# Kernel tuning notes

Measured on AMD Instinct MI355X. Metric: run time of the kernel, lower is better.

## Reference

```python
import jax, jax.numpy as jnp
import numpy as np

D_IN = 1024
D_H = 1024

def setup_inputs() -> dict:
    key = jax.random.key(0)
    ks = jax.random.split(key, 9)
    s = 1.0 / np.sqrt(D_IN)
    inp = {
        'x': jax.random.normal(ks[0], (4, 2048, D_IN), dtype=jnp.float32),
        'wq': jax.random.uniform(ks[1], (D_IN, D_H), jnp.float32, -s, s),
        'bq': jax.random.uniform(ks[2], (D_H,), jnp.float32, -s, s),
        'wk': jax.random.uniform(ks[3], (D_IN, D_H), jnp.float32, -s, s),
        'bk': jax.random.uniform(ks[4], (D_H,), jnp.float32, -s, s),
        'wv': jax.random.uniform(ks[5], (D_IN, D_H), jnp.float32, -s, s),
        'bv': jax.random.uniform(ks[6], (D_H,), jnp.float32, -s, s),
        'wo': jax.random.uniform(ks[7], (D_H, D_IN), jnp.float32, -s, s),
        'bo': jax.random.uniform(ks[8], (D_IN,), jnp.float32, -s, s),
    }
    return inp

def reference(x, wq, bq, wk, bk, wv, bv, wo, bo):
    # q,k,v: [b, s, d]
    q = x @ wq + bq
    k = x @ wk + bk
    v = x @ wv + bv
    scale = 1.0 / jnp.sqrt(jnp.asarray(D_H, x.dtype))
    attn = jnp.einsum('bqd,bkd->bqk', q, k) * scale  # [b, s, s]
    attn = jax.nn.softmax(attn, axis=-1)
    score = jnp.einsum('bqk,bkd->bqd', attn, v)
    out = score @ wo + bo
    return out
```

## Files before the change

### kernel.cpp

```cpp
#include <hip/hip_runtime.h>


typedef unsigned short u16;
typedef short bf16x8 __attribute__((ext_vector_type(8)));
typedef float f32x4 __attribute__((ext_vector_type(4)));

#define SEQ 2048
#define DIM 1024

__device__ __forceinline__ u16 f2bf(float f) {
    unsigned u = __builtin_bit_cast(unsigned, f);
    u += 0x7fffu + ((u >> 16) & 1u);
    return (u16)(u >> 16);
}

__device__ __forceinline__ void async16(void* lds, const void* gmem) {
    __builtin_amdgcn_global_load_lds(
        (const __attribute__((address_space(1))) void*)gmem,
        (__attribute__((address_space(3))) void*)lds, 16, 0, 0);
}

__global__ __launch_bounds__(256) void cast_x_kernel(
    const float* __restrict__ x, u16* __restrict__ xb,
    const float* __restrict__ bq, const float* __restrict__ bk,
    const float* __restrict__ bv, float* __restrict__ bqkv,
    float* __restrict__ l)
{
    const int b = blockIdx.x;
    if (b < 8192) {
        const int idx = b * 256 + threadIdx.x;
        float4 v = ((const float4*)x)[idx];
        ushort4 o;
        o.x = f2bf(v.x); o.y = f2bf(v.y); o.z = f2bf(v.z); o.w = f2bf(v.w);
        ((ushort4*)xb)[idx] = o;
    } else {
        const int i = (b - 8192) * 256 + threadIdx.x;
        if (i < 3072)
            bqkv[i] = (i < 1024) ? bq[i] : (i < 2048) ? bk[i - 1024] : bv[i - 2048];
        else if (i < 3072 + 8192)
            l[i - 3072] = 0.f;
    }
}

__global__ __launch_bounds__(256) void transpose_cast_all(
    const float* __restrict__ W0, const float* __restrict__ W1,
    const float* __restrict__ W2, const float* __restrict__ W3,
    u16* __restrict__ Tqkv, u16* __restrict__ To)
{
    __shared__ float tile[32][33];
    const int z = blockIdx.z;
    const float* W = (z == 0) ? W0 : (z == 1) ? W1 : (z == 2) ? W2 : W3;
    u16* T = (z < 3) ? (Tqkv + (size_t)z * 1048576) : To;

    const int bx = blockIdx.x * 32, by = blockIdx.y * 32;
    const int tx = threadIdx.x, ty = threadIdx.y;
    #pragma unroll
    for (int r = 0; r < 4; ++r)
        tile[ty + r * 8][tx] = W[(size_t)(by + ty + r * 8) * DIM + bx + tx];
    __syncthreads();
    #pragma unroll
    for (int r = 0; r < 4; ++r) {
        const float v = tile[tx][ty + r * 8];
        T[(size_t)(bx + ty + r * 8) * DIM + by + tx] = f2bf(v);
    }
}

#define EPI_BF16BIAS 0
#define EPI_BF16     1
#define EPI_ELOGIT   2
#define EPI_PVOUT    3

template<int EPI, int K, int LDA, int LDB, int LDC>
__global__ __launch_bounds__(128, 2) void gemm2w(
    const u16* __restrict__ A, const u16* __restrict__ Bt,
    const float* __restrict__ bias, u16* __restrict__ C,
    float* __restrict__ Cf, float* __restrict__ lsum,
    float scale, long sA, long sB, long sC)
{
    __shared__ u16 sA0[128 * 32], sB0[128 * 32];
    __shared__ u16 sA1[128 * 32], sB1[128 * 32];

    const int z = blockIdx.z;
    A  += (size_t)z * sA;
    Bt += (size_t)z * sB;

    const int t  = threadIdx.x;
    const int m0 = blockIdx.y * 128, n0 = blockIdx.x * 128;
    const int wv = t >> 6, lane = t & 63;
    const int wm = wv * 64;
    const int lrow = lane & 15, quad = lane >> 4;
    const int sw = quad ^ ((lrow >> 1) & 3);

    f32x4 acc[4][8];
    #pragma unroll
    for (int i = 0; i < 4; ++i)
        #pragma unroll
        for (int j = 0; j < 8; ++j)
            acc[i][j] = (f32x4){0.f, 0.f, 0.f, 0.f};

    auto stage = [&](u16* dA, u16* dB, int k0) {
        #pragma unroll
        for (int p = 0; p < 4; ++p) {
            const int slot = p * 128 + t;
            const int row  = slot >> 2;
            const int c8   = (slot & 3) ^ ((row >> 1) & 3);
            async16(&dA[slot * 8], &A[(size_t)(m0 + row) * LDA + k0 + c8 * 8]);
        }
        #pragma unroll
        for (int p = 0; p < 4; ++p) {
            const int slot = p * 128 + t;
            const int row  = slot >> 2;
            const int c8   = (slot & 3) ^ ((row >> 1) & 3);
            async16(&dB[slot * 8], &Bt[(size_t)(n0 + row) * LDB + k0 + c8 * 8]);
        }
    };
    auto compute = [&](const u16* bA, const u16* bB) {
        bf16x8 af[4], bf[8];
        #pragma unroll
        for (int i = 0; i < 4; ++i)
            af[i] = *(const bf16x8*)&bA[((wm + i * 16 + lrow) * 4 + sw) * 8];
        #pragma unroll
        for (int j = 0; j < 8; ++j)
            bf[j] = *(const bf16x8*)&bB[((j * 16 + lrow) * 4 + sw) * 8];
        #pragma unroll
        for (int i = 0; i < 4; ++i)
            #pragma unroll
            for (int j = 0; j < 8; ++j)
                acc[i][j] = __builtin_amdgcn_mfma_f32_16x16x32_bf16(
                    af[i], bf[j], acc[i][j], 0, 0, 0);
    };

    stage(sA0, sB0, 0);
    __syncthreads();
    #pragma unroll 1
    for (int k0 = 0; k0 + 64 < K; k0 += 64) {
        stage(sA1, sB1, k0 + 32);
        compute(sA0, sB0);
        __syncthreads();
        stage(sA0, sB0, k0 + 64);
        compute(sA1, sB1);
        __syncthreads();
    }
    stage(sA1, sB1, K - 32);
    compute(sA0, sB0);
    __syncthreads();
    compute(sA1, sB1);

    if (EPI == EPI_PVOUT) Cf += (size_t)z * sC;
    else                  C  += (size_t)z * sC;

    #pragma unroll
    for (int i = 0; i < 4; ++i) {
        const int row = m0 + wm + i * 16 + quad * 4;
        if (EPI == EPI_BF16BIAS) {
            #pragma unroll
            for (int j = 0; j < 8; ++j) {
                const int col = n0 + j * 16 + lrow;
                const float b = bias[col];
                const f32x4 a = acc[i][j];
                #pragma unroll
                for (int r = 0; r < 4; ++r)
                    C[(size_t)(row + r) * LDC + col] = f2bf(a[r] + b);
            }
        } else if (EPI == EPI_BF16) {
            #pragma unroll
            for (int j = 0; j < 8; ++j) {
                const int col = n0 + j * 16 + lrow;
                const f32x4 a = acc[i][j];
                #pragma unroll
                for (int r = 0; r < 4; ++r)
                    C[(size_t)(row + r) * LDC + col] = f2bf(a[r]);
            }
        } else if (EPI == EPI_ELOGIT) {
            float rs[4] = {0.f, 0.f, 0.f, 0.f};
            #pragma unroll
            for (int j = 0; j < 8; ++j) {
                const int col = n0 + j * 16 + lrow;
                const f32x4 a = acc[i][j];
                #pragma unroll
                for (int r = 0; r < 4; ++r) {
                    const float e = __expf(a[r] * scale);
                    C[(size_t)(row + r) * LDC + col] = f2bf(e);
                    rs[r] += e;
                }
            }
            #pragma unroll
            for (int r = 0; r < 4; ++r) {
                float s = rs[r];
                s += __shfl_xor(s, 1, 64);
                s += __shfl_xor(s, 2, 64);
                s += __shfl_xor(s, 4, 64);
                s += __shfl_xor(s, 8, 64);
                if (lrow == 0)
                    atomicAdd(&lsum[(size_t)z * 2048 + row + r], s);
            }
        } else {
            float linv[4];
            #pragma unroll
            for (int r = 0; r < 4; ++r)
                linv[r] = 1.0f / lsum[(size_t)z * 2048 + row + r];
            #pragma unroll
            for (int j = 0; j < 8; ++j) {
                const int col = n0 + j * 16 + lrow;
                const float b = bias[col];
                const f32x4 a = acc[i][j];
                #pragma unroll
                for (int r = 0; r < 4; ++r)
                    Cf[(size_t)(row + r) * LDC + col] = a[r] * linv[r] + b;
            }
        }
    }
}

extern "C" void kernel_launch(void* const* d_in, const int* in_sizes, int n_in,
                              void* d_out, int out_size, void* d_ws, size_t ws_size,
                              hipStream_t stream)
{
    const float* x  = (const float*)d_in[0];
    const float* wq = (const float*)d_in[1];
    const float* bq = (const float*)d_in[2];
    const float* wk = (const float*)d_in[3];
    const float* bk = (const float*)d_in[4];
    const float* wv = (const float*)d_in[5];
    const float* bv = (const float*)d_in[6];
    const float* wo = (const float*)d_in[7];
    const float* bo = (const float*)d_in[8];
    float* out = (float*)d_out;

    u16* w16   = (u16*)d_ws;
    u16* xb    = w16;
    u16* qkv   = w16 + 8388608;
    u16* E     = w16 + 33554432;
    u16* wqkvT = w16 + 50331648;
    u16* woT   = w16 + 53477376;
    float* bqkv = (float*)(w16 + 54525952);
    float* l    = (float*)(w16 + 54532096);
    u16* VWoT  = w16;

    const u16* q_ = qkv;
    const u16* k_ = qkv + 1024;
    const u16* v_ = qkv + 2048;

    cast_x_kernel<<<8236, dim3(256), 0, stream>>>(x, xb, bq, bk, bv, bqkv, l);
    transpose_cast_all<<<dim3(32, 32, 4), dim3(32, 8), 0, stream>>>(
        wq, wk, wv, wo, wqkvT, woT);

    gemm2w<EPI_BF16BIAS, 1024, 1024, 1024, 3072>
        <<<dim3(24, 64, 1), dim3(128), 0, stream>>>(
            xb, wqkvT, bqkv, qkv, nullptr, nullptr, 1.f, 0, 0, 0);

    gemm2w<EPI_ELOGIT, 1024, 3072, 3072, 2048>
        <<<dim3(16, 16, 4), dim3(128), 0, stream>>>(
            q_, k_, nullptr, E, nullptr, l, 0.03125f,
            6291456, 6291456, 4194304);

    gemm2w<EPI_BF16, 1024, 1024, 3072, 2048>
        <<<dim3(16, 8, 4), dim3(128), 0, stream>>>(
            woT, v_, nullptr, VWoT, nullptr, nullptr, 1.f,
            0, 6291456, 2097152);

    gemm2w<EPI_PVOUT, 2048, 2048, 2048, 1024>
        <<<dim3(8, 16, 4), dim3(128), 0, stream>>>(
            E, VWoT, bo, nullptr, out, l, 1.f,
            4194304, 2097152, 2097152);
}
```

Baseline: 305.5 us.

## Rewrite GEMM as 8-wave 256x256 tile kernel with staged async pipeline

The 2-wave 128x128 GEMM is replaced by an 8-wave kernel computing 256x256 output tiles with K=64 steps. Global-to-LDS copies are split into four half-tile stages, issued two tiles ahead and interleaved with four MFMA quadrants separated by barriers, with explicit vmcnt waits and s_setprio around the MFMA bursts. LDS uses an XOR swizzle. The goal is more reuse per loaded tile and better overlap of memory with matrix math. In exchange, grids shrink (e.g. 128-256 blocks), which may underfill the GPU's CUs, and the many barriers add synchronization overhead.

```diff
diff --git a/kernel.cpp b/kernel.cpp
--- a/kernel.cpp
+++ b/kernel.cpp
@@ -70,103 +70,162 @@
 #define EPI_ELOGIT   2
 #define EPI_PVOUT    3
 
+#define FENCE() asm volatile("" ::: "memory")
+
+#define MFMA_QUAD(mh, nh)                                                    \
+    do {                                                                     \
+        __builtin_amdgcn_s_setprio(1);                                       \
+        _Pragma("unroll")                                                    \
+        for (int ks = 0; ks < 2; ++ks)                                       \
+            _Pragma("unroll")                                                \
+            for (int q = 0; q < 4; ++q)                                      \
+                _Pragma("unroll")                                            \
+                for (int nn = 0; nn < 2; ++nn)                               \
+                    acc[(mh) * 4 + q][(nh) * 2 + nn] =                       \
+                        __builtin_amdgcn_mfma_f32_16x16x32_bf16(             \
+                            aF[q][ks], bF[(nh) * 2 + nn][ks],                \
+                            acc[(mh) * 4 + q][(nh) * 2 + nn], 0, 0, 0);      \
+        __builtin_amdgcn_s_setprio(0);                                       \
+    } while (0)
+
 template<int EPI, int K, int LDA, int LDB, int LDC>
-__global__ __launch_bounds__(128, 2) void gemm2w(
+__global__ __launch_bounds__(512, 2) void gemm8w(
     const u16* __restrict__ A, const u16* __restrict__ Bt,
     const float* __restrict__ bias, u16* __restrict__ C,
     float* __restrict__ Cf, float* __restrict__ lsum,
     float scale, long sA, long sB, long sC)
 {
-    __shared__ u16 sA0[128 * 32], sB0[128 * 32];
-    __shared__ u16 sA1[128 * 32], sB1[128 * 32];
+    __shared__ u16 lds[2][2][2][8192];
+
+    constexpr int NT = K / 64;
 
     const int z = blockIdx.z;
     A  += (size_t)z * sA;
     Bt += (size_t)z * sB;
 
-    const int t  = threadIdx.x;
-    const int m0 = blockIdx.y * 128, n0 = blockIdx.x * 128;
-    const int wv = t >> 6, lane = t & 63;
-    const int wm = wv * 64;
+    const int t = threadIdx.x;
+    const int wid = t >> 6, lane = t & 63;
+    const int wm = wid >> 2, wn = wid & 3;
     const int lrow = lane & 15, quad = lane >> 4;
-    const int sw = quad ^ ((lrow >> 1) & 3);
-
-    f32x4 acc[4][8];
-    #pragma unroll
-    for (int i = 0; i < 4; ++i)
-        #pragma unroll
-        for (int j = 0; j < 8; ++j)
+    const int m0 = blockIdx.y * 256, n0 = blockIdx.x * 256;
+
+    int ldsoff[2], offA[2], offB[2];
+    #pragma unroll
+    for (int p = 0; p < 2; ++p) {
+        const int L  = p * 8192 + wid * 1024 + lane * 16;
+        const int sL = L ^ (((L >> 7) & 7) << 4);
+        const int r  = sL >> 7;
+        const int c  = (sL & 127) >> 1;
+        ldsoff[p] = L;
+        offA[p]   = r * LDA + c;
+        offB[p]   = r * LDB + c;
+    }
+    const u16* ABase = A  + (size_t)m0 * LDA;
+    const u16* BBase = Bt + (size_t)n0 * LDB;
+
+    auto stage = [&](int tile, int sel) {
+        const int mat = sel >> 1, half = sel & 1, buf = tile & 1;
+        char* dst = (char*)&lds[buf][mat][half][0];
+        const int k0 = tile * 64;
+        #pragma unroll
+        for (int p = 0; p < 2; ++p) {
+            const u16* src = mat
+                ? BBase + (size_t)half * (128 * (size_t)LDB) + k0 + offB[p]
+                : ABase + (size_t)half * (128 * (size_t)LDA) + k0 + offA[p];
+            async16(dst + ldsoff[p], src);
+        }
+    };
+
+    f32x4 acc[8][4];
+    #pragma unroll
+    for (int i = 0; i < 8; ++i)
+        #pragma unroll
+        for (int j = 0; j < 4; ++j)
             acc[i][j] = (f32x4){0.f, 0.f, 0.f, 0.f};
 
-    auto stage = [&](u16* dA, u16* dB, int k0) {
-        #pragma unroll
-        for (int p = 0; p < 4; ++p) {
-            const int slot = p * 128 + t;
-            const int row  = slot >> 2;
-            const int c8   = (slot & 3) ^ ((row >> 1) & 3);
-            async16(&dA[slot * 8], &A[(size_t)(m0 + row) * LDA + k0 + c8 * 8]);
-        }
-        #pragma unroll
-        for (int p = 0; p < 4; ++p) {
-            const int slot = p * 128 + t;
-            const int row  = slot >> 2;
-            const int c8   = (slot & 3) ^ ((row >> 1) & 3);
-            async16(&dB[slot * 8], &Bt[(size_t)(n0 + row) * LDB + k0 + c8 * 8]);
-        }
+    bf16x8 aF[4][2], bF[4][2];
+
+    auto ldA1 = [&](int buf, int mi, int ks) -> bf16x8 {
+        int b = (mi * 16 + lrow) * 128 + ks * 64 + quad * 16;
+        b ^= ((b >> 7) & 7) << 4;
+        return *(const bf16x8*)((const char*)&lds[buf][0][wm][0] + b);
     };
-    auto compute = [&](const u16* bA, const u16* bB) {
-        bf16x8 af[4], bf[8];
-        #pragma unroll
-        for (int i = 0; i < 4; ++i)
-            af[i] = *(const bf16x8*)&bA[((wm + i * 16 + lrow) * 4 + sw) * 8];
-        #pragma unroll
-        for (int j = 0; j < 8; ++j)
-            bf[j] = *(const bf16x8*)&bB[((j * 16 + lrow) * 4 + sw) * 8];
-        #pragma unroll
-        for (int i = 0; i < 4; ++i)
-            #pragma unroll
-            for (int j = 0; j < 8; ++j)
-                acc[i][j] = __builtin_amdgcn_mfma_f32_16x16x32_bf16(
-                    af[i], bf[j], acc[i][j], 0, 0, 0);
+    auto ldB1 = [&](int buf, int ni, int ks) -> bf16x8 {
+        int b = ((wn & 1) * 64 + ni * 16 + lrow) * 128 + ks * 64 + quad * 16;
+        b ^= ((b >> 7) & 7) << 4;
+        return *(const bf16x8*)((const char*)&lds[buf][1][wn >> 1][0] + b);
     };
 
-    stage(sA0, sB0, 0);
-    __syncthreads();
+    stage(0, 0); stage(0, 1); stage(0, 2); stage(0, 3);
+    stage(1, 2); stage(1, 3); stage(1, 0);
+    asm volatile("s_waitcnt vmcnt(6)" ::: "memory");
+    __builtin_amdgcn_s_barrier();
+
     #pragma unroll 1
-    for (int k0 = 0; k0 + 64 < K; k0 += 64) {
-        stage(sA1, sB1, k0 + 32);
-        compute(sA0, sB0);
-        __syncthreads();
-        stage(sA0, sB0, k0 + 64);
-        compute(sA1, sB1);
-        __syncthreads();
-    }
-    stage(sA1, sB1, K - 32);
-    compute(sA0, sB0);
-    __syncthreads();
-    compute(sA1, sB1);
+    for (int T = 0; T < NT; ++T) {
+        const int buf = T & 1;
+        const bool s1 = (T + 1 < NT), s2 = (T + 2 < NT);
+
+        #pragma unroll
+        for (int q = 0; q < 4; ++q) {
+            aF[q][0] = ldA1(buf, q, 0);
+            aF[q][1] = ldA1(buf, q, 1);
+        }
+        #pragma unroll
+        for (int ni = 0; ni < 4; ++ni) {
+            bF[ni][0] = ldB1(buf, ni, 0);
+            bF[ni][1] = ldB1(buf, ni, 1);
+        }
+        if (s1) stage(T + 1, 1);
+        FENCE(); __builtin_amdgcn_s_barrier();
+        MFMA_QUAD(0, 0);
+        FENCE(); __builtin_amdgcn_s_barrier();
+
+        MFMA_QUAD(0, 1);
+        FENCE(); __builtin_amdgcn_s_barrier();
+
+        #pragma unroll
+        for (int q = 0; q < 4; ++q) {
+            aF[q][0] = ldA1(buf, 4 + q, 0);
+            aF[q][1] = ldA1(buf, 4 + q, 1);
+        }
+        if (s2) { stage(T + 2, 2); stage(T + 2, 3); }
+        FENCE(); __builtin_amdgcn_s_barrier();
+        MFMA_QUAD(1, 1);
+        FENCE(); __builtin_amdgcn_s_barrier();
+
+        if (s2) {
+            stage(T + 2, 0);
+            asm volatile("s_waitcnt vmcnt(6)" ::: "memory");
+        } else {
+            asm volatile("s_waitcnt vmcnt(0)" ::: "memory");
+        }
+        FENCE(); __builtin_amdgcn_s_barrier();
+        MFMA_QUAD(1, 0);
+        FENCE(); __builtin_amdgcn_s_barrier();
+    }
 
     if (EPI == EPI_PVOUT) Cf += (size_t)z * sC;
     else                  C  += (size_t)z * sC;
 
     #pragma unroll
-    for (int i = 0; i < 4; ++i) {
-        const int row = m0 + wm + i * 16 + quad * 4;
+    for (int mi = 0; mi < 8; ++mi) {
+        const int row = m0 + wm * 128 + mi * 16 + quad * 4;
         if (EPI == EPI_BF16BIAS) {
             #pragma unroll
-            for (int j = 0; j < 8; ++j) {
-                const int col = n0 + j * 16 + lrow;
-                const float b = bias[col];
-                const f32x4 a = acc[i][j];
+            for (int ni = 0; ni < 4; ++ni) {
+                const int col = n0 + wn * 64 + ni * 16 + lrow;
+                const float bb = bias[col];
+                const f32x4 a = acc[mi][ni];
                 #pragma unroll
                 for (int r = 0; r < 4; ++r)
-                    C[(size_t)(row + r) * LDC + col] = f2bf(a[r] + b);
+                    C[(size_t)(row + r) * LDC + col] = f2bf(a[r] + bb);
             }
         } else if (EPI == EPI_BF16) {
             #pragma unroll
-            for (int j = 0; j < 8; ++j) {
-                const int col = n0 + j * 16 + lrow;
-                const f32x4 a = acc[i][j];
+            for (int ni = 0; ni < 4; ++ni) {
+                const int col = n0 + wn * 64 + ni * 16 + lrow;
+                const f32x4 a = acc[mi][ni];
                 #pragma unroll
                 for (int r = 0; r < 4; ++r)
                     C[(size_t)(row + r) * LDC + col] = f2bf(a[r]);
@@ -174,9 +233,9 @@
         } else if (EPI == EPI_ELOGIT) {
             float rs[4] = {0.f, 0.f, 0.f, 0.f};
             #pragma unroll
-            for (int j = 0; j < 8; ++j) {
-                const int col = n0 + j * 16 + lrow;
-                const f32x4 a = acc[i][j];
+            for (int ni = 0; ni < 4; ++ni) {
+                const int col = n0 + wn * 64 + ni * 16 + lrow;
+                const f32x4 a = acc[mi][ni];
                 #pragma unroll
                 for (int r = 0; r < 4; ++r) {
                     const float e = __expf(a[r] * scale);
@@ -200,13 +259,13 @@
             for (int r = 0; r < 4; ++r)
                 linv[r] = 1.0f / lsum[(size_t)z * 2048 + row + r];
             #pragma unroll
-            for (int j = 0; j < 8; ++j) {
-                const int col = n0 + j * 16 + lrow;
-                const float b = bias[col];
-                const f32x4 a = acc[i][j];
+            for (int ni = 0; ni < 4; ++ni) {
+                const int col = n0 + wn * 64 + ni * 16 + lrow;
+                const float bb = bias[col];
+                const f32x4 a = acc[mi][ni];
                 #pragma unroll
                 for (int r = 0; r < 4; ++r)
-                    Cf[(size_t)(row + r) * LDC + col] = a[r] * linv[r] + b;
+                    Cf[(size_t)(row + r) * LDC + col] = a[r] * linv[r] + bb;
             }
         }
     }
@@ -245,22 +304,22 @@
     transpose_cast_all<<<dim3(32, 32, 4), dim3(32, 8), 0, stream>>>(
         wq, wk, wv, wo, wqkvT, woT);
 
-    gemm2w<EPI_BF16BIAS, 1024, 1024, 1024, 3072>
-        <<<dim3(24, 64, 1), dim3(128), 0, stream>>>(
+    gemm8w<EPI_BF16BIAS, 1024, 1024, 1024, 3072>
+        <<<dim3(12, 32, 1), dim3(512), 0, stream>>>(
             xb, wqkvT, bqkv, qkv, nullptr, nullptr, 1.f, 0, 0, 0);
 
-    gemm2w<EPI_ELOGIT, 1024, 3072, 3072, 2048>
-        <<<dim3(16, 16, 4), dim3(128), 0, stream>>>(
+    gemm8w<EPI_ELOGIT, 1024, 3072, 3072, 2048>
+        <<<dim3(8, 8, 4), dim3(512), 0, stream>>>(
             q_, k_, nullptr, E, nullptr, l, 0.03125f,
             6291456, 6291456, 4194304);
 
-    gemm2w<EPI_BF16, 1024, 1024, 3072, 2048>
-        <<<dim3(16, 8, 4), dim3(128), 0, stream>>>(
+    gemm8w<EPI_BF16, 1024, 1024, 3072, 2048>
+        <<<dim3(8, 4, 4), dim3(512), 0, stream>>>(
             woT, v_, nullptr, VWoT, nullptr, nullptr, 1.f,
             0, 6291456, 2097152);
 
-    gemm2w<EPI_PVOUT, 2048, 2048, 2048, 1024>
-        <<<dim3(8, 16, 4), dim3(128), 0, stream>>>(
+    gemm8w<EPI_PVOUT, 2048, 2048, 2048, 1024>
+        <<<dim3(4, 8, 4), dim3(512), 0, stream>>>(
             E, VWoT, bo, nullptr, out, l, 1.f,
             4194304, 2097152, 2097152);
 }
```

Measured after the change: 304.0 us. No clear change (-0.5%).
